# Kernel optimization log

Hardware: AMD Instinct MI355X
Metric: run time of the kernel (lower is better)

The kernel has to match this reference:

```python
import jax, jax.numpy as jnp
import numpy as np

B, S, D = 8, 1024, 768
H, DH = 8, 96          # number_of_heads, head_outdim = D // H
DFF = 4 * D            # mlp hidden
EPS = 1e-5


def _p(key, shape, scale=0.02):
    return (jax.random.normal(key, shape, dtype=jnp.float32) * scale)


def setup_inputs() -> dict:
    key = jax.random.key(0)
    ks = jax.random.split(key, 16)
    return {
        "h": jax.random.normal(ks[0], (B, S, D), dtype=jnp.float32),
        "x": jax.random.normal(ks[1], (B, S, D), dtype=jnp.float32),
        # SLN 1: scalar gamma/beta + LayerNorm affine
        "g1": jnp.ones((), jnp.float32), "be1": jnp.zeros((), jnp.float32),
        "ln1_w": jnp.ones((D,), jnp.float32), "ln1_b": jnp.zeros((D,), jnp.float32),
        # SLN 2
        "g2": jnp.ones((), jnp.float32), "be2": jnp.zeros((), jnp.float32),
        "ln2_w": jnp.ones((D,), jnp.float32), "ln2_b": jnp.zeros((D,), jnp.float32),
        # MSA projections (stored as [in, out] for x @ W)
        "Wq": _p(ks[2], (D, H * DH)), "bq": jnp.zeros((H * DH,), jnp.float32),
        "Wk": _p(ks[3], (D, H * DH)), "bk": jnp.zeros((H * DH,), jnp.float32),
        "Wv": _p(ks[4], (D, H * DH)), "bv": jnp.zeros((H * DH,), jnp.float32),
        "Wo": _p(ks[5], (H * DH, D)), "bo": jnp.zeros((D,), jnp.float32),
        # MLP: D -> 4D -> D, relu
        "W1": _p(ks[6], (D, DFF)), "b1": jnp.zeros((DFF,), jnp.float32),
        "W2": _p(ks[7], (DFF, D)), "b2": jnp.zeros((D,), jnp.float32),
    }


def _sln(h, x, gamma, beta, w, b):
    # SLN(h, x) = gamma * x * LayerNorm(h) + beta * x
    mu = jnp.mean(h, axis=-1, keepdims=True)
    var = jnp.var(h, axis=-1, keepdims=True)
    ln = (h - mu) * jax.lax.rsqrt(var + EPS) * w + b
    return gamma * x * ln + beta * x


def _l2_msa(h, Wq, bq, Wk, bk, Wv, bv, Wo, bo):
    # L2-distance multi-head self-attention (lp=2)
    def heads(W, bias):
        y = h @ W + bias                      # [B,S,H*DH]
        return y.reshape(B, S, H, DH).transpose(0, 2, 1, 3)  # [B,H,S,DH]
    q, k, v = heads(Wq, bq), heads(Wk, bk), heads(Wv, bv)
    # pairwise L2 distances via the quadratic expansion (avoids [B,H,S,S,DH])
    q2 = jnp.sum(q * q, axis=-1)              # [B,H,S]
    k2 = jnp.sum(k * k, axis=-1)              # [B,H,S]
    qk = jnp.einsum("bhsd,bhtd->bhst", q, k)  # [B,H,S,S]
    d2 = jnp.maximum(q2[..., :, None] + k2[..., None, :] - 2.0 * qk, 0.0)
    dist = jnp.sqrt(d2)                       # cdist(q, k, p=2)
    attn = jax.nn.softmax(-dist / np.sqrt(DH), axis=-1)
    out = jnp.einsum("bhst,bhtd->bhsd", attn, v)  # [B,H,S,DH]
    out = out.transpose(0, 2, 1, 3).reshape(B, S, H * DH)
    return out @ Wo + bo


def reference(h, x, g1, be1, ln1_w, ln1_b, g2, be2, ln2_w, ln2_b,
              Wq, bq, Wk, bk, Wv, bv, Wo, bo, W1, b1, W2, b2):
    h1 = _sln(h, x, g1, be1, ln1_w, ln1_b)
    htmp = _l2_msa(h1, Wq, bq, Wk, bk, Wv, bv, Wo, bo) + h   # dropout_rate=0 -> identity
    h2 = _sln(htmp, x, g2, be2, ln2_w, ln2_b)
    hf = jax.nn.relu(h2 @ W1 + b1) @ W2 + b2 + htmp
    return (x, hf)
```

## Files before the change

### kernel.cpp

```cpp
#include <hip/hip_runtime.h>
#include <math.h>

#define B_ 8
#define S_ 1024
#define D_ 768
#define H_ 8
#define DH_ 96
#define DFF_ 3072
#define NTOK (B_*S_)
#define QKVW 2304
#define EPS_ 1e-5f
#define CEXP_ 0.14724445f

typedef __attribute__((ext_vector_type(4))) float f4;
typedef __attribute__((ext_vector_type(4))) int i4;
typedef __attribute__((ext_vector_type(8))) __bf16 bf16x8;
typedef __attribute__((ext_vector_type(4))) unsigned short us4;
typedef __attribute__((ext_vector_type(8))) unsigned short us8;

static __device__ __forceinline__ unsigned short f2bf(float f) {
    unsigned int u = __builtin_bit_cast(unsigned int, f);
    u += 0x7fffu + ((u >> 16) & 1u);
    return (unsigned short)(u >> 16);
}
static __device__ __forceinline__ float bf2f(unsigned short u) {
    unsigned int x = ((unsigned int)u) << 16;
    return __builtin_bit_cast(float, x);
}

#define GLOBAL_LOAD_LDS16(g, l) \
    __builtin_amdgcn_global_load_lds((const __attribute__((address_space(1))) unsigned int*)(g), \
                                     (__attribute__((address_space(3))) unsigned int*)(l), 16, 0, 0)

__global__ __launch_bounds__(192) void sln_kernel(
    const float* __restrict__ h, const float* __restrict__ x,
    const float* __restrict__ gamma, const float* __restrict__ beta,
    const float* __restrict__ w, const float* __restrict__ bvec,
    unsigned short* __restrict__ out_bf, float* __restrict__ xcopy)
{
    int row = blockIdx.x;
    int t = threadIdx.x;
    const float4* h4 = (const float4*)(h + (size_t)row * D_);
    const float4* x4 = (const float4*)(x + (size_t)row * D_);
    float4 hv = h4[t];
    float s  = hv.x + hv.y + hv.z + hv.w;
    float ss = hv.x*hv.x + hv.y*hv.y + hv.z*hv.z + hv.w*hv.w;
    #pragma unroll
    for (int off = 32; off > 0; off >>= 1) {
        s  += __shfl_down(s, off);
        ss += __shfl_down(ss, off);
    }
    __shared__ float red[2][3];
    int wid = t >> 6;
    if ((t & 63) == 0) { red[0][wid] = s; red[1][wid] = ss; }
    __syncthreads();
    float sum   = red[0][0] + red[0][1] + red[0][2];
    float sumsq = red[1][0] + red[1][1] + red[1][2];
    float mu  = sum * (1.0f / D_);
    float var = sumsq * (1.0f / D_) - mu * mu;
    float rstd = rsqrtf(var + EPS_);
    float g = gamma[0], be = beta[0];
    float4 wv = ((const float4*)w)[t];
    float4 bv = ((const float4*)bvec)[t];
    float4 xv = x4[t];
    us4 o;
    o.x = f2bf(xv.x * (g * ((hv.x - mu) * rstd * wv.x + bv.x) + be));
    o.y = f2bf(xv.y * (g * ((hv.y - mu) * rstd * wv.y + bv.y) + be));
    o.z = f2bf(xv.z * (g * ((hv.z - mu) * rstd * wv.z + bv.z) + be));
    o.w = f2bf(xv.w * (g * ((hv.w - mu) * rstd * wv.w + bv.w) + be));
    *(us4*)(out_bf + (size_t)row * D_ + t * 4) = o;
    if (xcopy) ((float4*)(xcopy + (size_t)row * D_))[t] = xv;
}

__global__ __launch_bounds__(256) void prep_all_kernel(
    const float* __restrict__ Wq, const float* __restrict__ Wk,
    const float* __restrict__ Wv, const float* __restrict__ Wo,
    const float* __restrict__ W1, const float* __restrict__ W2,
    const float* __restrict__ bq, const float* __restrict__ bk, const float* __restrict__ bv,
    unsigned short* __restrict__ Wqkvt, unsigned short* __restrict__ Wot,
    unsigned short* __restrict__ W1t, unsigned short* __restrict__ W2t,
    float* __restrict__ bqkv)
{
    int id = blockIdx.x;
    int tx = threadIdx.x, ty = threadIdx.y;
    if (id >= 6912) {
        int i = (id - 6912) * 256 + ty * 32 + tx;
        if (i < QKVW) {
            float v = (i < 768) ? CEXP_ * bq[i]
                    : (i < 1536) ? -2.f * CEXP_ * bk[i - 768] : bv[i - 1536];
            bqkv[i] = v;
        }
        return;
    }
    const float* in; unsigned short* out; int K, N, nbx, rel;
    float scl = 1.f;
    if (id < 1728)      { int m = id / 576; rel = id % 576;
                          in = (m == 0) ? Wq : (m == 1) ? Wk : Wv;
                          if (m == 0) scl = CEXP_;
                          if (m == 1) scl = -2.f * CEXP_;
                          out = Wqkvt + (size_t)m * 768 * 768; K = 768; N = 768; nbx = 24; }
    else if (id < 2304) { rel = id - 1728; in = Wo; out = Wot;  K = 768;  N = 768;  nbx = 24; }
    else if (id < 4608) { rel = id - 2304; in = W1; out = W1t;  K = 768;  N = 3072; nbx = 96; }
    else                { rel = id - 4608; in = W2; out = W2t;  K = 3072; N = 768;  nbx = 24; }
    int n0 = (rel % nbx) * 32, k0 = (rel / nbx) * 32;
    __shared__ float tile[32][33];
    #pragma unroll
    for (int r = 0; r < 4; r++)
        tile[ty + r * 8][tx] = in[(size_t)(k0 + ty + r * 8) * N + n0 + tx];
    __syncthreads();
    #pragma unroll
    for (int r = 0; r < 4; r++)
        out[(size_t)(n0 + ty + r * 8) * K + k0 + tx] = f2bf(scl * tile[tx][ty + r * 8]);
}

template<int OUT_BF16, int RELU>
__global__ __launch_bounds__(256) void gemm_mfma_kernel(
    const unsigned short* __restrict__ A, const unsigned short* __restrict__ Bt,
    const float* __restrict__ bias, const float* __restrict__ resid,
    void* __restrict__ Cout, int M, int N, int K)
{
    __shared__ unsigned short Asm[2][128 * 32];
    __shared__ unsigned short Bsm[2][128 * 32];

    int t = threadIdx.x;
    int lane = t & 63, wv = t >> 6;
    int wm = wv & 1, wn = wv >> 1;
    int l16 = lane & 15, quad = lane >> 4;

    int bm = blockIdx.x * 128;
    int bn = blockIdx.y * 128;

    const unsigned short* Abase = A  + (size_t)bm * K;
    const unsigned short* Bbase = Bt + (size_t)bn * K;

    int fl0 = t, fl1 = 256 + t;
    int r0 = fl0 >> 2, lg0 = (fl0 ^ (fl0 >> 3)) & 3;
    int r1 = fl1 >> 2, lg1 = (fl1 ^ (fl1 >> 3)) & 3;

    f4 acc[4][4] = {};

    GLOBAL_LOAD_LDS16(Abase + (size_t)r0 * K + lg0 * 8, &Asm[0][fl0 * 8]);
    GLOBAL_LOAD_LDS16(Abase + (size_t)r1 * K + lg1 * 8, &Asm[0][fl1 * 8]);
    GLOBAL_LOAD_LDS16(Bbase + (size_t)r0 * K + lg0 * 8, &Bsm[0][fl0 * 8]);
    GLOBAL_LOAD_LDS16(Bbase + (size_t)r1 * K + lg1 * 8, &Bsm[0][fl1 * 8]);
    __syncthreads();

    int nk = K >> 5;
    int cur = 0;
    for (int it = 0; it < nk; ++it) {
        if (it + 1 < nk) {
            int k0 = (it + 1) << 5;
            GLOBAL_LOAD_LDS16(Abase + (size_t)r0 * K + k0 + lg0 * 8, &Asm[cur ^ 1][fl0 * 8]);
            GLOBAL_LOAD_LDS16(Abase + (size_t)r1 * K + k0 + lg1 * 8, &Asm[cur ^ 1][fl1 * 8]);
            GLOBAL_LOAD_LDS16(Bbase + (size_t)r0 * K + k0 + lg0 * 8, &Bsm[cur ^ 1][fl0 * 8]);
            GLOBAL_LOAD_LDS16(Bbase + (size_t)r1 * K + k0 + lg1 * 8, &Bsm[cur ^ 1][fl1 * 8]);
        }

        bf16x8 xf[4], wf[4];
        #pragma unroll
        for (int i = 0; i < 4; i++) {
            int m = wm * 64 + i * 16 + l16;
            int p = (quad ^ (m >> 1)) & 3;
            xf[i] = __builtin_bit_cast(bf16x8, *(const i4*)&Asm[cur][m * 32 + p * 8]);
        }
        #pragma unroll
        for (int j = 0; j < 4; j++) {
            int n = wn * 64 + j * 16 + l16;
            int p = (quad ^ (n >> 1)) & 3;
            wf[j] = __builtin_bit_cast(bf16x8, *(const i4*)&Bsm[cur][n * 32 + p * 8]);
        }
        #pragma unroll
        for (int j = 0; j < 4; j++)
            #pragma unroll
            for (int i = 0; i < 4; i++)
                acc[j][i] = __builtin_amdgcn_mfma_f32_16x16x32_bf16(wf[j], xf[i], acc[j][i], 0, 0, 0);

        __syncthreads();
        cur ^= 1;
    }

    #pragma unroll
    for (int i = 0; i < 4; i++) {
        int rowg = bm + wm * 64 + i * 16 + l16;
        #pragma unroll
        for (int j = 0; j < 4; j++) {
            int colg0 = bn + wn * 64 + j * 16 + quad * 4;
            f4 v = acc[j][i];
            f4 b4 = *(const f4*)&bias[colg0];
            v += b4;
            if (RELU) {
                #pragma unroll
                for (int r = 0; r < 4; r++) v[r] = fmaxf(v[r], 0.f);
            }
            if (resid) {
                f4 r4 = *(const f4*)&resid[(size_t)rowg * N + colg0];
                v += r4;
            }
            if (OUT_BF16) {
                us4 o;
                o.x = f2bf(v[0]); o.y = f2bf(v[1]); o.z = f2bf(v[2]); o.w = f2bf(v[3]);
                *(us4*)((unsigned short*)Cout + (size_t)rowg * N + colg0) = o;
            } else {
                *(f4*)((float*)Cout + (size_t)rowg * N + colg0) = v;
            }
        }
    }
}

template<int OUT_BF16, int RELU>
__global__ __launch_bounds__(256) void gemm_mfma_n64_kernel(
    const unsigned short* __restrict__ A, const unsigned short* __restrict__ Bt,
    const float* __restrict__ bias, const float* __restrict__ resid,
    void* __restrict__ Cout, int M, int N, int K)
{
    __shared__ unsigned short Asm[2][128 * 64];
    __shared__ unsigned short Bsm[2][64 * 64];

    int t = threadIdx.x;
    int lane = t & 63, wv = t >> 6;
    int wm = wv & 1, wn = wv >> 1;
    int l16 = lane & 15, quad = lane >> 4;

    int bm = blockIdx.x * 128;
    int bn = blockIdx.y * 64;

    const unsigned short* Abase = A  + (size_t)bm * K;
    const unsigned short* Bbase = Bt + (size_t)bn * K;

    int ar[4], alg[4], br[2], blg[2];
    #pragma unroll
    for (int i = 0; i < 4; i++) {
        int fl = t + i * 256;
        ar[i] = fl >> 3; alg[i] = (fl ^ (fl >> 3)) & 7;
    }
    #pragma unroll
    for (int i = 0; i < 2; i++) {
        int fl = t + i * 256;
        br[i] = fl >> 3; blg[i] = (fl ^ (fl >> 3)) & 7;
    }

    f4 acc[2][4] = {};

    #pragma unroll
    for (int i = 0; i < 4; i++)
        GLOBAL_LOAD_LDS16(Abase + (size_t)ar[i] * K + alg[i] * 8, &Asm[0][(t + i * 256) * 8]);
    #pragma unroll
    for (int i = 0; i < 2; i++)
        GLOBAL_LOAD_LDS16(Bbase + (size_t)br[i] * K + blg[i] * 8, &Bsm[0][(t + i * 256) * 8]);
    __syncthreads();

    int nk = K >> 6;
    int cur = 0;
    for (int it = 0; it < nk; ++it) {
        if (it + 1 < nk) {
            int k0 = (it + 1) << 6;
            #pragma unroll
            for (int i = 0; i < 4; i++)
                GLOBAL_LOAD_LDS16(Abase + (size_t)ar[i] * K + k0 + alg[i] * 8, &Asm[cur ^ 1][(t + i * 256) * 8]);
            #pragma unroll
            for (int i = 0; i < 2; i++)
                GLOBAL_LOAD_LDS16(Bbase + (size_t)br[i] * K + k0 + blg[i] * 8, &Bsm[cur ^ 1][(t + i * 256) * 8]);
        }

        #pragma unroll
        for (int kk = 0; kk < 2; kk++) {
            bf16x8 xf[4], wf[2];
            #pragma unroll
            for (int i = 0; i < 4; i++) {
                int m = wm * 64 + i * 16 + l16;
                int p = ((kk * 4 + quad) ^ (m & 7)) & 7;
                xf[i] = __builtin_bit_cast(bf16x8, *(const i4*)&Asm[cur][m * 64 + p * 8]);
            }
            #pragma unroll
            for (int j = 0; j < 2; j++) {
                int n = wn * 32 + j * 16 + l16;
                int p = ((kk * 4 + quad) ^ (n & 7)) & 7;
                wf[j] = __builtin_bit_cast(bf16x8, *(const i4*)&Bsm[cur][n * 64 + p * 8]);
            }
            #pragma unroll
            for (int j = 0; j < 2; j++)
                #pragma unroll
                for (int i = 0; i < 4; i++)
                    acc[j][i] = __builtin_amdgcn_mfma_f32_16x16x32_bf16(wf[j], xf[i], acc[j][i], 0, 0, 0);
        }

        __syncthreads();
        cur ^= 1;
    }

    #pragma unroll
    for (int i = 0; i < 4; i++) {
        int rowg = bm + wm * 64 + i * 16 + l16;
        #pragma unroll
        for (int j = 0; j < 2; j++) {
            int colg0 = bn + wn * 32 + j * 16 + quad * 4;
            f4 v = acc[j][i];
            f4 b4 = *(const f4*)&bias[colg0];
            v += b4;
            if (RELU) {
                #pragma unroll
                for (int r = 0; r < 4; r++) v[r] = fmaxf(v[r], 0.f);
            }
            if (resid) {
                f4 r4 = *(const f4*)&resid[(size_t)rowg * N + colg0];
                v += r4;
            }
            if (OUT_BF16) {
                us4 o;
                o.x = f2bf(v[0]); o.y = f2bf(v[1]); o.z = f2bf(v[2]); o.w = f2bf(v[3]);
                *(us4*)((unsigned short*)Cout + (size_t)rowg * N + colg0) = o;
            } else {
                *(f4*)((float*)Cout + (size_t)rowg * N + colg0) = v;
            }
        }
    }
}

__global__ __launch_bounds__(256) void vtrans_norms_kernel(
    const unsigned short* __restrict__ qkv, unsigned short* __restrict__ vt,
    float* __restrict__ q2g, float* __restrict__ k2g)
{
    __shared__ unsigned short Vl[64][100];
    int blk = blockIdx.x;
    int bh = blk >> 4, kt = blk & 15;
    int b = bh >> 3, hh = bh & 7;
    int t = threadIdx.x;
    int key = t >> 2, qc = t & 3;
    const unsigned short* tok = qkv + ((size_t)(b * S_ + kt * 64 + key)) * QKVW + hh * DH_;
    float qs = 0.f, ks = 0.f;
    #pragma unroll
    for (int i = 0; i < 3; i++) {
        us8 qv = *(const us8*)(tok + (qc * 3 + i) * 8);
        us8 kv = *(const us8*)(tok + 768 + (qc * 3 + i) * 8);
        #pragma unroll
        for (int e = 0; e < 8; e++) {
            float qf = bf2f(qv[e]), kf = bf2f(kv[e]);
            qs += qf * qf; ks += kf * kf;
        }
    }
    qs += __shfl_xor(qs, 1, 4); qs += __shfl_xor(qs, 2, 4);
    ks += __shfl_xor(ks, 1, 4); ks += __shfl_xor(ks, 2, 4);
    if (qc == 0) {
        int idx = (b * H_ + hh) * S_ + kt * 64 + key;
        q2g[idx] = qs; k2g[idx] = ks * 0.25f;
    }
    const unsigned short* src = tok + 1536;
    #pragma unroll
    for (int i = 0; i < 3; i++) {
        int chunk = qc + i * 4;
        us8 v = *(const us8*)(src + chunk * 8);
        #pragma unroll
        for (int e = 0; e < 8; e++) Vl[key][chunk * 8 + e] = v[e];
    }
    __syncthreads();
    unsigned short* dst = vt + (size_t)blk * 7168;
    #pragma unroll
    for (int r = 0; r < 3; r++) {
        int c = r * 256 + t;
        int vd = c >> 3, kc = c & 7;
        us8 o;
        #pragma unroll
        for (int j = 0; j < 8; j++) o[j] = Vl[kc * 8 + j][vd];
        *(us8*)(dst + vd * 72 + kc * 8) = o;
    }
}

__global__ __launch_bounds__(256, 2) void attn_mfma_kernel(
    const unsigned short* __restrict__ qkv,
    const unsigned short* __restrict__ vt,
    const float* __restrict__ q2g, const float* __restrict__ k2g,
    unsigned short* __restrict__ outb)
{
    __shared__ unsigned short Klds[2][6144];
    __shared__ unsigned short Vlds[2][7168];
    __shared__ float k2lds[2][64];
    __shared__ unsigned short Plds[4][2][16 * 72];

    int t = threadIdx.x;
    int lane = t & 63, w = t >> 6;
    int l16 = lane & 15, quad = lane >> 4;

    int bid = blockIdx.x;
    int slot = bid >> 3;
    int bh = (bid & 7) * 8 + (slot >> 3);
    int qt = slot & 7;
    int b = bh >> 3, hh = bh & 7;

    int qrowW = qt * 128 + w * 32;

    const unsigned short* qb = qkv + ((size_t)(b * S_ + qrowW)) * QKVW + hh * DH_;
    bf16x8 qf[2][3];
    #pragma unroll
    for (int f = 0; f < 2; f++)
        #pragma unroll
        for (int d = 0; d < 3; d++)
            qf[f][d] = __builtin_bit_cast(bf16x8,
                *(const i4*)(qb + (size_t)(f * 16 + l16) * QKVW + d * 32 + quad * 8));

    float q2n[2];
    #pragma unroll
    for (int f = 0; f < 2; f++)
        q2n[f] = q2g[bh * S_ + qrowW + f * 16 + l16];

    float lsum0 = 0.f, lsum1 = 0.f;
    f4 Oacc[2][6] = {};

    const unsigned short* kgb = qkv + ((size_t)(b * S_)) * QKVW + 768 + hh * DH_;
    const unsigned short* vgb0 = vt + (size_t)(bh * 16) * 7168;
    const float* k2base = k2g + bh * S_;

    int kkey = t & 63;
    #define ATTN_STAGE(bb, itv)                                                   \
        {                                                                         \
            _Pragma("unroll")                                                     \
            for (int r = 0; r < 3; r++) {                                         \
                int c = r * 256 + t;                                              \
                int dc = c >> 6;                                                  \
                GLOBAL_LOAD_LDS16(kgb + ((size_t)((itv) * 64 + kkey)) * QKVW + dc * 8, \
                                  &Klds[bb][c * 8]);                              \
            }                                                                     \
            const unsigned short* vgb = vgb0 + (size_t)(itv) * 7168;              \
            _Pragma("unroll")                                                     \
            for (int r = 0; r < 3; r++)                                           \
                GLOBAL_LOAD_LDS16(vgb + (r * 256 + t) * 8, &Vlds[bb][(r * 256 + t) * 8]); \
            if (t < 128)                                                          \
                GLOBAL_LOAD_LDS16(vgb + (768 + t) * 8, &Vlds[bb][(768 + t) * 8]); \
            if (t < 16)                                                           \
                GLOBAL_LOAD_LDS16(k2base + (itv) * 64 + t * 4, &k2lds[bb][t * 4]); \
        }

    ATTN_STAGE(0, 0);
    __syncthreads();

    for (int it = 0; it < 16; it++) {
        int cur = it & 1;
        if (it) __syncthreads();
        if (it + 1 < 16) ATTN_STAGE(cur ^ 1, it + 1);

        const unsigned short* kB = &Klds[cur][quad * 512 + l16 * 8];
        #pragma unroll
        for (int kt2 = 0; kt2 < 4; kt2++) {
            const unsigned short* kp = kB + kt2 * 128;
            bf16x8 kf0 = __builtin_bit_cast(bf16x8, *(const i4*)(kp));
            bf16x8 kf1 = __builtin_bit_cast(bf16x8, *(const i4*)(kp + 2048));
            bf16x8 kf2 = __builtin_bit_cast(bf16x8, *(const i4*)(kp + 4096));
            f4 kk = *(const f4*)&k2lds[cur][kt2 * 16 + quad * 4];
            #pragma unroll
            for (int f = 0; f < 2; f++) {
                f4 a = {kk[0] + q2n[f], kk[1] + q2n[f], kk[2] + q2n[f], kk[3] + q2n[f]};
                __builtin_amdgcn_s_setprio(1);
                a = __builtin_amdgcn_mfma_f32_16x16x32_bf16(kf0, qf[f][0], a, 0, 0, 0);
                a = __builtin_amdgcn_mfma_f32_16x16x32_bf16(kf1, qf[f][1], a, 0, 0, 0);
                a = __builtin_amdgcn_mfma_f32_16x16x32_bf16(kf2, qf[f][2], a, 0, 0, 0);
                __builtin_amdgcn_s_setprio(0);
                #pragma unroll
                for (int r2 = 0; r2 < 4; r2++) {
                    float p = exp2f(-__builtin_amdgcn_sqrtf(__builtin_fabsf(a[r2])));
                    if (f == 0) lsum0 += p; else lsum1 += p;
                    a[r2] = p;
                }
                unsigned int plo, phi;
                asm("v_cvt_pk_bf16_f32 %0, %1, %2" : "=v"(plo) : "v"(a[0]), "v"(a[1]));
                asm("v_cvt_pk_bf16_f32 %0, %1, %2" : "=v"(phi) : "v"(a[2]), "v"(a[3]));
                uint2 pkd; pkd.x = plo; pkd.y = phi;
                *(uint2*)&Plds[w][f][l16 * 72 + kt2 * 16 + quad * 4] = pkd;
            }
        }
        bf16x8 pa[2][2];
        #pragma unroll
        for (int f = 0; f < 2; f++) {
            pa[f][0] = __builtin_bit_cast(bf16x8, *(const i4*)&Plds[w][f][l16 * 72 + quad * 8]);
            pa[f][1] = __builtin_bit_cast(bf16x8, *(const i4*)&Plds[w][f][l16 * 72 + 32 + quad * 8]);
        }
        __builtin_amdgcn_s_setprio(1);
        #pragma unroll
        for (int vtl = 0; vtl < 6; vtl++) {
            bf16x8 vf0 = __builtin_bit_cast(bf16x8, *(const i4*)&Vlds[cur][(vtl * 16 + l16) * 72 + quad * 8]);
            bf16x8 vf1 = __builtin_bit_cast(bf16x8, *(const i4*)&Vlds[cur][(vtl * 16 + l16) * 72 + 32 + quad * 8]);
            #pragma unroll
            for (int f = 0; f < 2; f++) {
                Oacc[f][vtl] = __builtin_amdgcn_mfma_f32_16x16x32_bf16(pa[f][0], vf0, Oacc[f][vtl], 0, 0, 0);
                Oacc[f][vtl] = __builtin_amdgcn_mfma_f32_16x16x32_bf16(pa[f][1], vf1, Oacc[f][vtl], 0, 0, 0);
            }
        }
        __builtin_amdgcn_s_setprio(0);
    }
    #pragma unroll
    for (int f = 0; f < 2; f++) {
        float ls = (f == 0) ? lsum0 : lsum1;
        ls += __shfl_xor(ls, 16, 64);
        ls += __shfl_xor(ls, 32, 64);
        float inv_l = 1.f / ls;
        f4 iv;
        #pragma unroll
        for (int r2 = 0; r2 < 4; r2++)
            iv[r2] = __shfl(inv_l, quad * 4 + r2, 64);
        #pragma unroll
        for (int vtl = 0; vtl < 6; vtl++)
            #pragma unroll
            for (int r2 = 0; r2 < 4; r2++) {
                int row = b * S_ + qrowW + f * 16 + quad * 4 + r2;
                outb[(size_t)row * D_ + hh * DH_ + vtl * 16 + l16] = f2bf(Oacc[f][vtl][r2] * iv[r2]);
            }
    }
    #undef ATTN_STAGE
}

extern "C" void kernel_launch(void* const* d_in, const int* in_sizes, int n_in,
                              void* d_out, int out_size, void* d_ws, size_t ws_size,
                              hipStream_t stream)
{
    const float* h    = (const float*)d_in[0];
    const float* x    = (const float*)d_in[1];
    const float* g1   = (const float*)d_in[2];
    const float* be1  = (const float*)d_in[3];
    const float* ln1w = (const float*)d_in[4];
    const float* ln1b = (const float*)d_in[5];
    const float* g2   = (const float*)d_in[6];
    const float* be2  = (const float*)d_in[7];
    const float* ln2w = (const float*)d_in[8];
    const float* ln2b = (const float*)d_in[9];
    const float* Wq   = (const float*)d_in[10];
    const float* bq   = (const float*)d_in[11];
    const float* Wk   = (const float*)d_in[12];
    const float* bk   = (const float*)d_in[13];
    const float* Wv   = (const float*)d_in[14];
    const float* bv   = (const float*)d_in[15];
    const float* Wo   = (const float*)d_in[16];
    const float* bo   = (const float*)d_in[17];
    const float* W1   = (const float*)d_in[18];
    const float* b1   = (const float*)d_in[19];
    const float* W2   = (const float*)d_in[20];
    const float* b2   = (const float*)d_in[21];

    float* out = (float*)d_out;
    char* wsb = (char*)d_ws;
    const size_t ND = (size_t)NTOK * D_;

    size_t off = 0;
    unsigned short* W1t = (unsigned short*)(wsb + off); off += 4718592;
    unsigned short* W2t = (unsigned short*)(wsb + off); off += 4718592;
    float* bqkv = (float*)(wsb + off);                  off += 16384;
    float* htmp = (float*)(wsb + off);                  off += ND * 4;
    float* q2g  = (float*)(wsb + off);                  off += (size_t)B_ * H_ * S_ * 4;
    float* k2g  = (float*)(wsb + off);                  off += (size_t)B_ * H_ * S_ * 4;
    unsigned short* h2b = (unsigned short*)(wsb + off); off += ND * 2;
    size_t pool0 = off;
    unsigned short* Wqkvt = (unsigned short*)(wsb + off); off += 3538944;
    unsigned short* Wot   = (unsigned short*)(wsb + off); off += 1179648;
    unsigned short* h1b   = (unsigned short*)(wsb + off); off += ND * 2;
    unsigned short* vtg   = (unsigned short*)(wsb + off); off += (size_t)1024 * 14336;
    unsigned short* qkvb  = (unsigned short*)(wsb + off); off += (size_t)NTOK * QKVW * 2;
    unsigned short* attnb   = h1b;
    unsigned short* hiddenb = (unsigned short*)(wsb + pool0);

    prep_all_kernel<<<6921, dim3(32, 8), 0, stream>>>(
        Wq, Wk, Wv, Wo, W1, W2, bq, bk, bv, Wqkvt, Wot, W1t, W2t, bqkv);

    sln_kernel<<<NTOK, 192, 0, stream>>>(h, x, g1, be1, ln1w, ln1b, h1b, out);

    gemm_mfma_kernel<1, 0><<<dim3(NTOK/128, QKVW/128), 256, 0, stream>>>(
        h1b, Wqkvt, bqkv, nullptr, qkvb, NTOK, QKVW, D_);

    vtrans_norms_kernel<<<1024, 256, 0, stream>>>(qkvb, vtg, q2g, k2g);

    attn_mfma_kernel<<<512, 256, 0, stream>>>(qkvb, vtg, q2g, k2g, attnb);

    gemm_mfma_n64_kernel<0, 0><<<dim3(NTOK/128, D_/64), 256, 0, stream>>>(
        attnb, Wot, bo, h, htmp, NTOK, D_, D_);

    sln_kernel<<<NTOK, 192, 0, stream>>>(htmp, x, g2, be2, ln2w, ln2b, h2b, nullptr);

    gemm_mfma_kernel<1, 1><<<dim3(NTOK/128, DFF_/128), 256, 0, stream>>>(
        h2b, W1t, b1, nullptr, hiddenb, NTOK, DFF_, D_);
    gemm_mfma_n64_kernel<0, 0><<<dim3(NTOK/128, D_/64), 256, 0, stream>>>(
        hiddenb, W2t, b2, htmp, out + ND, NTOK, D_, DFF_);

    (void)in_sizes; (void)n_in; (void)out_size; (void)ws_size;
}
```

Measured before the change: 404.7 us.

## Triple-buffer GEMM LDS tiles with fine-grained vmcnt waits

Changes the MFMA GEMM from a double-buffered to a triple-buffered LDS pipeline that prefetches two K-tiles ahead. It replaces __syncthreads with explicit s_waitcnt vmcnt(4) plus s_barrier, so only the oldest stage's loads must land before each iteration. This aims to hide more global-load latency behind the MFMA work. In exchange LDS use per block rises by half, which may cut occupancy. The stage is also issued after the fragment reads, so the buffer-reuse ordering depends on the barrier.

```diff
diff --git a/kernel.cpp b/kernel.cpp
--- a/kernel.cpp
+++ b/kernel.cpp
@@ -119,8 +119,8 @@
     const float* __restrict__ bias, const float* __restrict__ resid,
     void* __restrict__ Cout, int M, int N, int K)
 {
-    __shared__ unsigned short Asm[2][128 * 32];
-    __shared__ unsigned short Bsm[2][128 * 32];
+    __shared__ unsigned short Asm[3][128 * 32];
+    __shared__ unsigned short Bsm[3][128 * 32];
 
     int t = threadIdx.x;
     int lane = t & 63, wv = t >> 6;
@@ -139,23 +139,23 @@
 
     f4 acc[4][4] = {};
 
-    GLOBAL_LOAD_LDS16(Abase + (size_t)r0 * K + lg0 * 8, &Asm[0][fl0 * 8]);
-    GLOBAL_LOAD_LDS16(Abase + (size_t)r1 * K + lg1 * 8, &Asm[0][fl1 * 8]);
-    GLOBAL_LOAD_LDS16(Bbase + (size_t)r0 * K + lg0 * 8, &Bsm[0][fl0 * 8]);
-    GLOBAL_LOAD_LDS16(Bbase + (size_t)r1 * K + lg1 * 8, &Bsm[0][fl1 * 8]);
-    __syncthreads();
+    #define GSTAGE(s, kt)                                                        \
+        {                                                                        \
+            int k0_ = (kt) << 5;                                                 \
+            GLOBAL_LOAD_LDS16(Abase + (size_t)r0 * K + k0_ + lg0 * 8, &Asm[s][fl0 * 8]); \
+            GLOBAL_LOAD_LDS16(Abase + (size_t)r1 * K + k0_ + lg1 * 8, &Asm[s][fl1 * 8]); \
+            GLOBAL_LOAD_LDS16(Bbase + (size_t)r0 * K + k0_ + lg0 * 8, &Bsm[s][fl0 * 8]); \
+            GLOBAL_LOAD_LDS16(Bbase + (size_t)r1 * K + k0_ + lg1 * 8, &Bsm[s][fl1 * 8]); \
+        }
 
     int nk = K >> 5;
+    GSTAGE(0, 0);
+    GSTAGE(1, 1);
+    asm volatile("s_waitcnt vmcnt(4)" ::: "memory");
+    __builtin_amdgcn_s_barrier();
+
     int cur = 0;
     for (int it = 0; it < nk; ++it) {
-        if (it + 1 < nk) {
-            int k0 = (it + 1) << 5;
-            GLOBAL_LOAD_LDS16(Abase + (size_t)r0 * K + k0 + lg0 * 8, &Asm[cur ^ 1][fl0 * 8]);
-            GLOBAL_LOAD_LDS16(Abase + (size_t)r1 * K + k0 + lg1 * 8, &Asm[cur ^ 1][fl1 * 8]);
-            GLOBAL_LOAD_LDS16(Bbase + (size_t)r0 * K + k0 + lg0 * 8, &Bsm[cur ^ 1][fl0 * 8]);
-            GLOBAL_LOAD_LDS16(Bbase + (size_t)r1 * K + k0 + lg1 * 8, &Bsm[cur ^ 1][fl1 * 8]);
-        }
-
         bf16x8 xf[4], wf[4];
         #pragma unroll
         for (int i = 0; i < 4; i++) {
@@ -169,15 +169,24 @@
             int p = (quad ^ (n >> 1)) & 3;
             wf[j] = __builtin_bit_cast(bf16x8, *(const i4*)&Bsm[cur][n * 32 + p * 8]);
         }
+
+        if (it + 2 < nk) {
+            int nxt = cur + 2; if (nxt >= 3) nxt -= 3;
+            GSTAGE(nxt, it + 2);
+        }
+
         #pragma unroll
         for (int j = 0; j < 4; j++)
             #pragma unroll
             for (int i = 0; i < 4; i++)
                 acc[j][i] = __builtin_amdgcn_mfma_f32_16x16x32_bf16(wf[j], xf[i], acc[j][i], 0, 0, 0);
 
-        __syncthreads();
-        cur ^= 1;
-    }
+        if (it + 2 < nk) asm volatile("s_waitcnt vmcnt(4)" ::: "memory");
+        else             asm volatile("s_waitcnt vmcnt(0)" ::: "memory");
+        __builtin_amdgcn_s_barrier();
+        cur = (cur + 1 == 3) ? 0 : cur + 1;
+    }
+    #undef GSTAGE
 
     #pragma unroll
     for (int i = 0; i < 4; i++) {
```

New measurement: 406.6 us. Within noise of the previous version (+0.5%).

## Split attention block into 8 waves of 16 query rows each

Applied to the files above, without the earlier changes.

The attention kernel now launches 512 threads per block, each of 8 waves handling 16 query rows instead of 4 waves handling 32. The K/V staging loads are spread across the larger thread count. The aim is more waves in flight per block and less register pressure per wave, which should help hide latency in the softmax and MFMA loop. The cost is that each K/V fragment read from LDS is now reused across only one query fragment instead of two, so LDS read traffic per MFMA doubles.

```diff
diff --git a/kernel.cpp b/kernel.cpp
--- a/kernel.cpp
+++ b/kernel.cpp
@@ -365,7 +365,7 @@
     }
 }
 
-__global__ __launch_bounds__(256, 2) void attn_mfma_kernel(
+__global__ __launch_bounds__(512, 4) void attn_mfma_kernel(
     const unsigned short* __restrict__ qkv,
     const unsigned short* __restrict__ vt,
     const float* __restrict__ q2g, const float* __restrict__ k2g,
@@ -374,7 +374,7 @@
     __shared__ unsigned short Klds[2][6144];
     __shared__ unsigned short Vlds[2][7168];
     __shared__ float k2lds[2][64];
-    __shared__ unsigned short Plds[4][2][16 * 72];
+    __shared__ unsigned short Plds[8][16 * 72];
 
     int t = threadIdx.x;
     int lane = t & 63, w = t >> 6;
@@ -386,45 +386,41 @@
     int qt = slot & 7;
     int b = bh >> 3, hh = bh & 7;
 
-    int qrowW = qt * 128 + w * 32;
+    int qrowW = qt * 128 + w * 16;
 
     const unsigned short* qb = qkv + ((size_t)(b * S_ + qrowW)) * QKVW + hh * DH_;
-    bf16x8 qf[2][3];
-    #pragma unroll
-    for (int f = 0; f < 2; f++)
-        #pragma unroll
-        for (int d = 0; d < 3; d++)
-            qf[f][d] = __builtin_bit_cast(bf16x8,
-                *(const i4*)(qb + (size_t)(f * 16 + l16) * QKVW + d * 32 + quad * 8));
-
-    float q2n[2];
-    #pragma unroll
-    for (int f = 0; f < 2; f++)
-        q2n[f] = q2g[bh * S_ + qrowW + f * 16 + l16];
-
-    float lsum0 = 0.f, lsum1 = 0.f;
-    f4 Oacc[2][6] = {};
+    bf16x8 qf[3];
+    #pragma unroll
+    for (int d = 0; d < 3; d++)
+        qf[d] = __builtin_bit_cast(bf16x8,
+            *(const i4*)(qb + (size_t)l16 * QKVW + d * 32 + quad * 8));
+
+    float q2n = q2g[bh * S_ + qrowW + l16];
+
+    float lsum = 0.f;
+    f4 Oacc[6] = {};
 
     const unsigned short* kgb = qkv + ((size_t)(b * S_)) * QKVW + 768 + hh * DH_;
     const unsigned short* vgb0 = vt + (size_t)(bh * 16) * 7168;
     const float* k2base = k2g + bh * S_;
 
-    int kkey = t & 63;
     #define ATTN_STAGE(bb, itv)                                                   \
         {                                                                         \
-            _Pragma("unroll")                                                     \
-            for (int r = 0; r < 3; r++) {                                         \
-                int c = r * 256 + t;                                              \
-                int dc = c >> 6;                                                  \
-                GLOBAL_LOAD_LDS16(kgb + ((size_t)((itv) * 64 + kkey)) * QKVW + dc * 8, \
+            {                                                                     \
+                int key = t & 63, dc = t >> 6;                                    \
+                GLOBAL_LOAD_LDS16(kgb + ((size_t)((itv) * 64 + key)) * QKVW + dc * 8, \
+                                  &Klds[bb][t * 8]);                              \
+            }                                                                     \
+            if (t < 256) {                                                        \
+                int c = 512 + t;                                                  \
+                int key = c & 63, dc = c >> 6;                                    \
+                GLOBAL_LOAD_LDS16(kgb + ((size_t)((itv) * 64 + key)) * QKVW + dc * 8, \
                                   &Klds[bb][c * 8]);                              \
             }                                                                     \
             const unsigned short* vgb = vgb0 + (size_t)(itv) * 7168;              \
-            _Pragma("unroll")                                                     \
-            for (int r = 0; r < 3; r++)                                           \
-                GLOBAL_LOAD_LDS16(vgb + (r * 256 + t) * 8, &Vlds[bb][(r * 256 + t) * 8]); \
-            if (t < 128)                                                          \
-                GLOBAL_LOAD_LDS16(vgb + (768 + t) * 8, &Vlds[bb][(768 + t) * 8]); \
+            GLOBAL_LOAD_LDS16(vgb + t * 8, &Vlds[bb][t * 8]);                     \
+            if (t < 384)                                                          \
+                GLOBAL_LOAD_LDS16(vgb + (512 + t) * 8, &Vlds[bb][(512 + t) * 8]); \
             if (t < 16)                                                           \
                 GLOBAL_LOAD_LDS16(k2base + (itv) * 64 + t * 4, &k2lds[bb][t * 4]); \
         }
@@ -445,64 +441,50 @@
             bf16x8 kf1 = __builtin_bit_cast(bf16x8, *(const i4*)(kp + 2048));
             bf16x8 kf2 = __builtin_bit_cast(bf16x8, *(const i4*)(kp + 4096));
             f4 kk = *(const f4*)&k2lds[cur][kt2 * 16 + quad * 4];
-            #pragma unroll
-            for (int f = 0; f < 2; f++) {
-                f4 a = {kk[0] + q2n[f], kk[1] + q2n[f], kk[2] + q2n[f], kk[3] + q2n[f]};
-                __builtin_amdgcn_s_setprio(1);
-                a = __builtin_amdgcn_mfma_f32_16x16x32_bf16(kf0, qf[f][0], a, 0, 0, 0);
-                a = __builtin_amdgcn_mfma_f32_16x16x32_bf16(kf1, qf[f][1], a, 0, 0, 0);
-                a = __builtin_amdgcn_mfma_f32_16x16x32_bf16(kf2, qf[f][2], a, 0, 0, 0);
-                __builtin_amdgcn_s_setprio(0);
-                #pragma unroll
-                for (int r2 = 0; r2 < 4; r2++) {
-                    float p = exp2f(-__builtin_amdgcn_sqrtf(__builtin_fabsf(a[r2])));
-                    if (f == 0) lsum0 += p; else lsum1 += p;
-                    a[r2] = p;
-                }
-                unsigned int plo, phi;
-                asm("v_cvt_pk_bf16_f32 %0, %1, %2" : "=v"(plo) : "v"(a[0]), "v"(a[1]));
-                asm("v_cvt_pk_bf16_f32 %0, %1, %2" : "=v"(phi) : "v"(a[2]), "v"(a[3]));
-                uint2 pkd; pkd.x = plo; pkd.y = phi;
-                *(uint2*)&Plds[w][f][l16 * 72 + kt2 * 16 + quad * 4] = pkd;
-            }
-        }
-        bf16x8 pa[2][2];
-        #pragma unroll
-        for (int f = 0; f < 2; f++) {
-            pa[f][0] = __builtin_bit_cast(bf16x8, *(const i4*)&Plds[w][f][l16 * 72 + quad * 8]);
-            pa[f][1] = __builtin_bit_cast(bf16x8, *(const i4*)&Plds[w][f][l16 * 72 + 32 + quad * 8]);
-        }
+            f4 a = {kk[0] + q2n, kk[1] + q2n, kk[2] + q2n, kk[3] + q2n};
+            __builtin_amdgcn_s_setprio(1);
+            a = __builtin_amdgcn_mfma_f32_16x16x32_bf16(kf0, qf[0], a, 0, 0, 0);
+            a = __builtin_amdgcn_mfma_f32_16x16x32_bf16(kf1, qf[1], a, 0, 0, 0);
+            a = __builtin_amdgcn_mfma_f32_16x16x32_bf16(kf2, qf[2], a, 0, 0, 0);
+            __builtin_amdgcn_s_setprio(0);
+            #pragma unroll
+            for (int r2 = 0; r2 < 4; r2++) {
+                float p = exp2f(-__builtin_amdgcn_sqrtf(__builtin_fabsf(a[r2])));
+                lsum += p;
+                a[r2] = p;
+            }
+            unsigned int plo, phi;
+            asm("v_cvt_pk_bf16_f32 %0, %1, %2" : "=v"(plo) : "v"(a[0]), "v"(a[1]));
+            asm("v_cvt_pk_bf16_f32 %0, %1, %2" : "=v"(phi) : "v"(a[2]), "v"(a[3]));
+            uint2 pkd; pkd.x = plo; pkd.y = phi;
+            *(uint2*)&Plds[w][l16 * 72 + kt2 * 16 + quad * 4] = pkd;
+        }
+        bf16x8 pa0 = __builtin_bit_cast(bf16x8, *(const i4*)&Plds[w][l16 * 72 + quad * 8]);
+        bf16x8 pa1 = __builtin_bit_cast(bf16x8, *(const i4*)&Plds[w][l16 * 72 + 32 + quad * 8]);
         __builtin_amdgcn_s_setprio(1);
         #pragma unroll
         for (int vtl = 0; vtl < 6; vtl++) {
             bf16x8 vf0 = __builtin_bit_cast(bf16x8, *(const i4*)&Vlds[cur][(vtl * 16 + l16) * 72 + quad * 8]);
             bf16x8 vf1 = __builtin_bit_cast(bf16x8, *(const i4*)&Vlds[cur][(vtl * 16 + l16) * 72 + 32 + quad * 8]);
-            #pragma unroll
-            for (int f = 0; f < 2; f++) {
-                Oacc[f][vtl] = __builtin_amdgcn_mfma_f32_16x16x32_bf16(pa[f][0], vf0, Oacc[f][vtl], 0, 0, 0);
-                Oacc[f][vtl] = __builtin_amdgcn_mfma_f32_16x16x32_bf16(pa[f][1], vf1, Oacc[f][vtl], 0, 0, 0);
-            }
+            Oacc[vtl] = __builtin_amdgcn_mfma_f32_16x16x32_bf16(pa0, vf0, Oacc[vtl], 0, 0, 0);
+            Oacc[vtl] = __builtin_amdgcn_mfma_f32_16x16x32_bf16(pa1, vf1, Oacc[vtl], 0, 0, 0);
         }
         __builtin_amdgcn_s_setprio(0);
     }
-    #pragma unroll
-    for (int f = 0; f < 2; f++) {
-        float ls = (f == 0) ? lsum0 : lsum1;
-        ls += __shfl_xor(ls, 16, 64);
-        ls += __shfl_xor(ls, 32, 64);
-        float inv_l = 1.f / ls;
-        f4 iv;
-        #pragma unroll
-        for (int r2 = 0; r2 < 4; r2++)
-            iv[r2] = __shfl(inv_l, quad * 4 + r2, 64);
-        #pragma unroll
-        for (int vtl = 0; vtl < 6; vtl++)
-            #pragma unroll
-            for (int r2 = 0; r2 < 4; r2++) {
-                int row = b * S_ + qrowW + f * 16 + quad * 4 + r2;
-                outb[(size_t)row * D_ + hh * DH_ + vtl * 16 + l16] = f2bf(Oacc[f][vtl][r2] * iv[r2]);
-            }
-    }
+    lsum += __shfl_xor(lsum, 16, 64);
+    lsum += __shfl_xor(lsum, 32, 64);
+    float inv_l = 1.f / lsum;
+    f4 iv;
+    #pragma unroll
+    for (int r2 = 0; r2 < 4; r2++)
+        iv[r2] = __shfl(inv_l, quad * 4 + r2, 64);
+    #pragma unroll
+    for (int vtl = 0; vtl < 6; vtl++)
+        #pragma unroll
+        for (int r2 = 0; r2 < 4; r2++) {
+            int row = b * S_ + qrowW + quad * 4 + r2;
+            outb[(size_t)row * D_ + hh * DH_ + vtl * 16 + l16] = f2bf(Oacc[vtl][r2] * iv[r2]);
+        }
     #undef ATTN_STAGE
 }
 
@@ -564,7 +546,7 @@
 
     vtrans_norms_kernel<<<1024, 256, 0, stream>>>(qkvb, vtg, q2g, k2g);
 
-    attn_mfma_kernel<<<512, 256, 0, stream>>>(qkvb, vtg, q2g, k2g, attnb);
+    attn_mfma_kernel<<<512, 512, 0, stream>>>(qkvb, vtg, q2g, k2g, attnb);
 
     gemm_mfma_n64_kernel<0, 0><<<dim3(NTOK/128, D_/64), 256, 0, stream>>>(
         attnb, Wot, bo, h, htmp, NTOK, D_, D_);
```

After: 416.8 us. +3.0%, slower.
